# Optimization experiments

Hardware: AMD Instinct MI355X
Metric: run time of the kernel (lower is better)

Reference implementation:

```python
import jax, jax.numpy as jnp
import numpy as np

NUM_HEADS = 8      # in_channels // num_head_channels = 512 // 64
NUM_GROUPS = 32    # GroupNorm groups
EPS = 1e-5


def setup_inputs() -> dict:
    key = jax.random.key(0)
    ks = jax.random.split(key, 6)
    C = 512
    x = jax.random.normal(ks[0], (8, C, 32, 32), dtype=jnp.float32)
    gn_w = jax.random.normal(ks[1], (C,), dtype=jnp.float32) * 0.1 + 1.0
    gn_b = jax.random.normal(ks[2], (C,), dtype=jnp.float32) * 0.1
    qkv_w = jax.random.normal(ks[3], (3 * C, C), dtype=jnp.float32) / np.sqrt(C)
    qkv_b = jnp.zeros((3 * C,), dtype=jnp.float32)
    # NOTE: original zero-initializes to_out; we use small random weights so the
    # attention path contributes to the output (math is identical).
    out_w = jax.random.normal(ks[4], (C, C), dtype=jnp.float32) * 0.02
    out_b = jax.random.normal(ks[5], (C,), dtype=jnp.float32) * 0.02
    return {"x": x, "gn_w": gn_w, "gn_b": gn_b, "qkv_w": qkv_w,
            "qkv_b": qkv_b, "out_w": out_w, "out_b": out_b}


def _group_norm(net, gn_w, gn_b):
    b, c, t = net.shape
    g = net.reshape(b, NUM_GROUPS, c // NUM_GROUPS, t)
    mu = jnp.mean(g, axis=(2, 3), keepdims=True)
    var = jnp.var(g, axis=(2, 3), keepdims=True)
    n = ((g - mu) * jax.lax.rsqrt(var + EPS)).reshape(b, c, t)
    return n * gn_w[None, :, None] + gn_b[None, :, None]


def reference(x, gn_w, gn_b, qkv_w, qkv_b, out_w, out_b):
    b, c, h, w = x.shape
    area = h * w
    inp = x.reshape(b, c, area)                      # [b, c, t]
    n = _group_norm(inp, gn_w, gn_b)
    # 1x1 conv1d == channel GEMM
    qkv = jnp.einsum('oc,bct->bot', qkv_w, n) + qkv_b[None, :, None]  # [b, 3c, t]
    hd = c // NUM_HEADS
    # split_qkv_after_heads: view(b*H, 3*hd, area) then split along channel
    qkv = qkv.reshape(b * NUM_HEADS, 3 * hd, area)
    q, k, v = qkv[:, :hd], qkv[:, hd:2 * hd], qkv[:, 2 * hd:]
    scale = 1.0 / np.sqrt(np.sqrt(hd))               # sqrt-sqrt per-tensor scale
    attn = jnp.einsum('bct,bcs->bts', q * scale, k * scale)  # [bH, t, s]
    prob = jax.nn.softmax(attn, axis=-1)
    net = jnp.einsum('bts,bcs->bct', prob, v).reshape(b, c, area)
    out = jnp.einsum('oc,bct->bot', out_w, net) + out_b[None, :, None]
    return (inp + out).reshape(b, c, h, w)
```

## Files before the change

### kernel.cpp

```cpp
#include <hip/hip_runtime.h>
#include <hip/hip_bf16.h>

typedef __bf16 bf16_t;
typedef __bf16 bf16x8 __attribute__((ext_vector_type(8)));
typedef __bf16 bf16x4 __attribute__((ext_vector_type(4)));
typedef short  s16x4  __attribute__((ext_vector_type(4)));
typedef float  f32x4  __attribute__((ext_vector_type(4)));

#define B_DIM 8
#define C_DIM 512
#define T_DIM 1024
#define NH 8
#define HD 64

#define QSCALE 0.180336880111112f

__device__ __forceinline__ f32x4 mfma16_bf16(bf16x4 a, bf16x4 b, f32x4 c) {
    return __builtin_amdgcn_mfma_f32_16x16x16bf16_1k(
        __builtin_bit_cast(s16x4, a), __builtin_bit_cast(s16x4, b), c, 0, 0, 0);
}

__device__ __forceinline__ void block_sync_lds() {
    asm volatile("s_waitcnt lgkmcnt(0)" ::: "memory");
    __builtin_amdgcn_s_barrier();
}

__global__ __launch_bounds__(256) void gn_kernel(const float* __restrict__ x,
                                                 const float* __restrict__ gw,
                                                 const float* __restrict__ gb,
                                                 bf16_t* __restrict__ n_t,
                                                 const float* __restrict__ w1,
                                                 const float* __restrict__ w2,
                                                 bf16_t* __restrict__ o1,
                                                 bf16_t* __restrict__ o2)
{
    __shared__ bf16_t sX[16384];
    __shared__ float sred[8];
    int tid = threadIdx.x;

    if (blockIdx.x >= 256) {
        int tid2 = (blockIdx.x - 256) * 256 + tid;
        for (int p = 0; p < 16; ++p) {
            int q = tid2 + p * 16384;
            const f32x4* src;
            bf16x4* dst;
            int qq;
            if (q < 196608) { src = (const f32x4*)w1; dst = (bf16x4*)o1; qq = q; }
            else            { src = (const f32x4*)w2; dst = (bf16x4*)o2; qq = q - 196608; }
            f32x4 f = src[qq];
            bf16x4 h;
            for (int j = 0; j < 4; ++j) h[j] = (bf16_t)f[j];
            dst[qq] = h;
        }
        return;
    }

    int bb  = blockIdx.x >> 5;
    int g   = blockIdx.x & 31;
    const f32x4* xg4 = reinterpret_cast<const f32x4*>(x + (size_t)(bb * C_DIM + g * 16) * T_DIM);

    float s = 0.f, sq = 0.f;
    for (int i = 0; i < 16; ++i) {
        int v = tid + i * 256;
        f32x4 f = xg4[v];
        bf16x4 h;
        for (int j = 0; j < 4; ++j) {
            s += f[j]; sq += f[j] * f[j];
            h[j] = (bf16_t)f[j];
        }
        *reinterpret_cast<bf16x4*>(sX + v * 4) = h;
    }
    for (int off = 1; off < 64; off <<= 1) {
        s  += __shfl_xor(s, off);
        sq += __shfl_xor(sq, off);
    }
    int wv = tid >> 6;
    if ((tid & 63) == 0) { sred[wv * 2] = s; sred[wv * 2 + 1] = sq; }
    __syncthreads();
    s  = sred[0] + sred[2] + sred[4] + sred[6];
    sq = sred[1] + sred[3] + sred[5] + sred[7];
    float mean = s * (1.f / 16384.f);
    float var  = sq * (1.f / 16384.f) - mean * mean;
    float rs   = rsqrtf(var + 1e-5f);

    int hf = tid & 1;
    float aa[8], bbias[8];
    for (int j = 0; j < 8; ++j) {
        int c = hf * 8 + j;
        float av = gw[g * 16 + c] * rs;
        aa[j] = av;
        bbias[j] = gb[g * 16 + c] - mean * av;
    }
    bf16_t* ob = n_t + (size_t)bb * T_DIM * C_DIM + g * 16 + hf * 8;
    for (int p = 0; p < 8; ++p) {
        int t = (tid >> 1) + p * 128;
        bf16x8 o;
        for (int j = 0; j < 8; ++j) {
            float xv = (float)sX[(hf * 8 + j) * 1024 + t];
            o[j] = (bf16_t)(xv * aa[j] + bbias[j]);
        }
        *reinterpret_cast<bf16x8*>(ob + (size_t)t * C_DIM) = o;
    }
}

__global__ __launch_bounds__(256, 4) void qkv_gemm_kernel(
    const bf16_t* __restrict__ wqb, const float* __restrict__ bq,
    const bf16_t* __restrict__ n_t, bf16_t* __restrict__ qkv)
{
    __shared__ bf16_t sA[128 * 72];
    __shared__ bf16_t sB[128 * 72];
    int tid = threadIdx.x;
    int w = tid >> 6, lane = tid & 63, quad = lane >> 4, l15 = lane & 15;
    int bx = blockIdx.x;
    int t0 = blockIdx.y * 128;
    int bb = blockIdx.z;
    int o0 = bx * 128;
    const bf16_t* Ab = wqb + (size_t)o0 * C_DIM;
    const bf16_t* Bb = n_t + ((size_t)bb * T_DIM + t0) * C_DIM;

    f32x4 acc[4][4];
    for (int mt = 0; mt < 4; ++mt)
        for (int nt = 0; nt < 4; ++nt)
            acc[mt][nt] = f32x4{0.f, 0.f, 0.f, 0.f};
    int mw0 = (w >> 1) * 64;
    int nw0 = (w & 1) * 64;

    for (int k0 = 0; k0 < C_DIM; k0 += 64) {
        for (int i = 0; i < 4; ++i) {
            int v = tid + i * 256;
            int row = v >> 3, c8 = v & 7;
            *reinterpret_cast<bf16x8*>(sA + row * 72 + c8 * 8) =
                *reinterpret_cast<const bf16x8*>(Ab + (size_t)row * C_DIM + k0 + c8 * 8);
        }
        for (int i = 0; i < 4; ++i) {
            int v = tid + i * 256;
            int row = v >> 3, c8 = v & 7;
            *reinterpret_cast<bf16x8*>(sB + row * 72 + c8 * 8) =
                *reinterpret_cast<const bf16x8*>(Bb + (size_t)row * C_DIM + k0 + c8 * 8);
        }
        __syncthreads();
        for (int kk = 0; kk < 2; ++kk) {
            bf16x8 af[4], bfr[4];
            for (int mt = 0; mt < 4; ++mt)
                af[mt] = *reinterpret_cast<const bf16x8*>(sA + (mw0 + mt * 16 + l15) * 72 + kk * 32 + quad * 8);
            for (int nt = 0; nt < 4; ++nt)
                bfr[nt] = *reinterpret_cast<const bf16x8*>(sB + (nw0 + nt * 16 + l15) * 72 + kk * 32 + quad * 8);
            for (int mt = 0; mt < 4; ++mt)
                for (int nt = 0; nt < 4; ++nt)
                    acc[mt][nt] = __builtin_amdgcn_mfma_f32_16x16x32_bf16(af[mt], bfr[nt], acc[mt][nt], 0, 0, 0);
        }
        __syncthreads();
    }

    for (int half = 0; half < 2; ++half) {
        int chunk = bx * 2 + half;
        int h = chunk / 3, type = chunk % 3;
        size_t base = ((size_t)(bb * NH + h) * 3 + type) * (64 * 1024);
        bool mine = (mw0 >> 6) == half;

        if (type < 2) {
            float scl = (type == 0) ? QSCALE : 1.0f;
            if (mine)
                for (int mt = 0; mt < 4; ++mt)
                    for (int nt = 0; nt < 4; ++nt)
                        for (int r = 0; r < 4; ++r) {
                            int mw = mt * 16 + quad * 4 + r;
                            int tl = nw0 + nt * 16 + l15;
                            float v = (acc[mt][nt][r] + bq[o0 + half * 64 + mw]) * scl;
                            sB[tl * 72 + mw] = (bf16_t)v;
                        }
            __syncthreads();
            for (int i = 0; i < 4; ++i) {
                int v = tid + i * 256;
                int tl = v >> 3, c8 = v & 7;
                bf16x8 d = *reinterpret_cast<const bf16x8*>(sB + tl * 72 + c8 * 8);
                *reinterpret_cast<bf16x8*>(qkv + base + (size_t)(t0 + tl) * 64 + c8 * 8) = d;
            }
            __syncthreads();
        } else {
            if (mine)
                for (int mt = 0; mt < 4; ++mt)
                    for (int nt = 0; nt < 4; ++nt)
                        for (int r = 0; r < 4; ++r) {
                            int mw = mt * 16 + quad * 4 + r;
                            int tl = nw0 + nt * 16 + l15;
                            float v = acc[mt][nt][r] + bq[o0 + half * 64 + mw];
                            sB[mw * 136 + tl] = (bf16_t)v;
                        }
            __syncthreads();
            for (int i = 0; i < 4; ++i) {
                int v = tid + i * 256;
                int cc = v >> 4, t8 = (v & 15) * 8;
                bf16x8 d = *reinterpret_cast<const bf16x8*>(sB + cc * 136 + t8);
                *reinterpret_cast<bf16x8*>(qkv + base + (size_t)cc * 1024 + t0 + t8) = d;
            }
            __syncthreads();
        }
    }
}

__global__ __launch_bounds__(256, 2) void attn_kernel(const bf16_t* __restrict__ qkv,
                                                      bf16_t* __restrict__ net_t)
{
    __shared__ bf16_t sK[4][64 * 72];
    __shared__ bf16_t sV[4][64 * 72];
    int tid = threadIdx.x;
    int w = tid >> 6, lane = tid & 63, quad = lane >> 4, l15 = lane & 15;
    int bh = blockIdx.x;
    int qt = blockIdx.y;
    size_t qb = (size_t)bh * 3 * 65536;
    const bf16_t* Qg = qkv + qb + (size_t)qt * 8192;
    const bf16_t* Kg = qkv + qb + 65536;
    const bf16_t* Vg = qkv + qb + 2 * 65536;

    bf16x8 qf[2][2];
    for (int tt = 0; tt < 2; ++tt)
        for (int kk = 0; kk < 2; ++kk)
            qf[tt][kk] = *reinterpret_cast<const bf16x8*>(
                Qg + (size_t)(tt * 64 + w * 16 + l15) * 64 + kk * 32 + quad * 8);

    int vrow = tid >> 3;
    int vcol = (tid & 7) * 8;

    bf16x8 kA[2], vA[2], kB[2], vB[2];

    auto load_tiles = [&](bf16x8* kr, bf16x8* vr, int s0) {
        for (int i = 0; i < 2; ++i) {
            int r = vrow + i * 32;
            kr[i] = *reinterpret_cast<const bf16x8*>(Kg + (size_t)(s0 + r) * 64 + vcol);
            vr[i] = *reinterpret_cast<const bf16x8*>(Vg + (size_t)r * 1024 + s0 + vcol);
        }
    };
    auto write_tiles = [&](bf16_t* sKb, bf16_t* sVb, const bf16x8* kr, const bf16x8* vr) {
        for (int i = 0; i < 2; ++i) {
            int r = vrow + i * 32;
            *reinterpret_cast<bf16x8*>(sKb + r * 72 + vcol) = kr[i];
            *reinterpret_cast<bf16x8*>(sVb + r * 72 + vcol) = vr[i];
        }
    };

    f32x4 O0[4], O1[4];
    for (int i = 0; i < 4; ++i) {
        O0[i] = f32x4{0.f, 0.f, 0.f, 0.f};
        O1[i] = f32x4{0.f, 0.f, 0.f, 0.f};
    }
    f32x4 L0 = f32x4{0.f, 0.f, 0.f, 0.f};
    f32x4 L1 = f32x4{0.f, 0.f, 0.f, 0.f};
    const bf16x4 kONES = bf16x4{(bf16_t)1.f, (bf16_t)1.f, (bf16_t)1.f, (bf16_t)1.f};

    auto compute_tile = [&](const bf16_t* sKb, const bf16_t* sVb) {
        __builtin_amdgcn_s_setprio(1);
        for (int mt = 0; mt < 4; ++mt) {
            const bf16_t* krow = sKb + (mt * 16 + l15) * 72 + quad * 8;
            bf16x8 kf0 = *reinterpret_cast<const bf16x8*>(krow);
            bf16x8 kf1 = *reinterpret_cast<const bf16x8*>(krow + 32);
            f32x4 S0 = f32x4{0.f, 0.f, 0.f, 0.f};
            f32x4 S1 = f32x4{0.f, 0.f, 0.f, 0.f};
            S0 = __builtin_amdgcn_mfma_f32_16x16x32_bf16(kf0, qf[0][0], S0, 0, 0, 0);
            S1 = __builtin_amdgcn_mfma_f32_16x16x32_bf16(kf0, qf[1][0], S1, 0, 0, 0);
            S0 = __builtin_amdgcn_mfma_f32_16x16x32_bf16(kf1, qf[0][1], S0, 0, 0, 0);
            S1 = __builtin_amdgcn_mfma_f32_16x16x32_bf16(kf1, qf[1][1], S1, 0, 0, 0);
            bf16x4 pf0, pf1;
            for (int r = 0; r < 4; ++r) {
                pf0[r] = (bf16_t)__builtin_amdgcn_exp2f(S0[r]);
                pf1[r] = (bf16_t)__builtin_amdgcn_exp2f(S1[r]);
            }
            L0 = mfma16_bf16(kONES, pf0, L0);
            L1 = mfma16_bf16(kONES, pf1, L1);
            for (int ct = 0; ct < 4; ++ct) {
                bf16x4 vf = *reinterpret_cast<const bf16x4*>(sVb + (ct * 16 + l15) * 72 + mt * 16 + quad * 4);
                O0[ct] = mfma16_bf16(vf, pf0, O0[ct]);
                O1[ct] = mfma16_bf16(vf, pf1, O1[ct]);
            }
        }
        __builtin_amdgcn_s_setprio(0);
    };

    load_tiles(kA, vA, 0);
    load_tiles(kB, vB, 64);
    write_tiles(sK[0], sV[0], kA, vA);
    write_tiles(sK[1], sV[1], kB, vB);
    load_tiles(kA, vA, 128);
    load_tiles(kB, vB, 192);
    block_sync_lds();

    for (int ep = 0; ep < 4; ++ep) {
        write_tiles(sK[2], sV[2], kA, vA);
        write_tiles(sK[3], sV[3], kB, vB);
        if (ep < 3) {
            load_tiles(kA, vA, (4 * ep + 4) * 64);
            load_tiles(kB, vB, (4 * ep + 5) * 64);
        }
        compute_tile(sK[0], sV[0]);
        compute_tile(sK[1], sV[1]);
        block_sync_lds();
        if (ep < 3) {
            write_tiles(sK[0], sV[0], kA, vA);
            write_tiles(sK[1], sV[1], kB, vB);
            load_tiles(kA, vA, (4 * ep + 6) * 64);
            load_tiles(kB, vB, (4 * ep + 7) * 64);
        }
        compute_tile(sK[2], sV[2]);
        compute_tile(sK[3], sV[3]);
        if (ep < 3) block_sync_lds();
    }

    float inv0 = 1.f / L0[0];
    float inv1 = 1.f / L1[0];

    int bb = bh >> 3, h = bh & 7;
    int tbase = qt * 128 + w * 16 + l15;
    bf16_t* orow0 = net_t + ((size_t)bb * T_DIM + tbase) * C_DIM + h * 64;
    bf16_t* orow1 = net_t + ((size_t)bb * T_DIM + tbase + 64) * C_DIM + h * 64;
    for (int ct = 0; ct < 4; ++ct) {
        bf16x4 o4, o5;
        for (int r = 0; r < 4; ++r) {
            o4[r] = (bf16_t)(O0[ct][r] * inv0);
            o5[r] = (bf16_t)(O1[ct][r] * inv1);
        }
        *reinterpret_cast<bf16x4*>(orow0 + ct * 16 + quad * 4) = o4;
        *reinterpret_cast<bf16x4*>(orow1 + ct * 16 + quad * 4) = o5;
    }
}

__global__ __launch_bounds__(256) void out_gemm_kernel(
    const bf16_t* __restrict__ wob, const float* __restrict__ bo,
    const bf16_t* __restrict__ net_t, const float* __restrict__ x,
    float* __restrict__ out)
{
    __shared__ bf16_t sA[64 * 72];
    __shared__ bf16_t sB[128 * 72];
    int tid = threadIdx.x;
    int w = tid >> 6, lane = tid & 63, quad = lane >> 4, l15 = lane & 15;
    int o0 = blockIdx.x * 64;
    int t0 = blockIdx.y * 128;
    int bb = blockIdx.z;
    const bf16_t* Ab = wob + (size_t)o0 * C_DIM;
    const bf16_t* Bb = net_t + ((size_t)bb * T_DIM + t0) * C_DIM;

    f32x4 acc[2][4];
    for (int mt = 0; mt < 2; ++mt)
        for (int nt = 0; nt < 4; ++nt)
            acc[mt][nt] = f32x4{0.f, 0.f, 0.f, 0.f};
    int mw0 = (w >> 1) * 32;
    int nw0 = (w & 1) * 64;

    for (int k0 = 0; k0 < C_DIM; k0 += 64) {
        for (int i = 0; i < 2; ++i) {
            int v = tid + i * 256;
            int row = v >> 3, c8 = v & 7;
            *reinterpret_cast<bf16x8*>(sA + row * 72 + c8 * 8) =
                *reinterpret_cast<const bf16x8*>(Ab + (size_t)row * C_DIM + k0 + c8 * 8);
        }
        for (int i = 0; i < 4; ++i) {
            int v = tid + i * 256;
            int row = v >> 3, c8 = v & 7;
            *reinterpret_cast<bf16x8*>(sB + row * 72 + c8 * 8) =
                *reinterpret_cast<const bf16x8*>(Bb + (size_t)row * C_DIM + k0 + c8 * 8);
        }
        __syncthreads();
        for (int kk = 0; kk < 2; ++kk) {
            bf16x8 af[2], bfr[4];
            for (int mt = 0; mt < 2; ++mt)
                af[mt] = *reinterpret_cast<const bf16x8*>(sA + (mw0 + mt * 16 + l15) * 72 + kk * 32 + quad * 8);
            for (int nt = 0; nt < 4; ++nt)
                bfr[nt] = *reinterpret_cast<const bf16x8*>(sB + (nw0 + nt * 16 + l15) * 72 + kk * 32 + quad * 8);
            for (int mt = 0; mt < 2; ++mt)
                for (int nt = 0; nt < 4; ++nt)
                    acc[mt][nt] = __builtin_amdgcn_mfma_f32_16x16x32_bf16(af[mt], bfr[nt], acc[mt][nt], 0, 0, 0);
        }
        __syncthreads();
    }

    for (int mt = 0; mt < 2; ++mt)
        for (int nt = 0; nt < 4; ++nt)
            for (int r = 0; r < 4; ++r) {
                int o = o0 + mw0 + mt * 16 + quad * 4 + r;
                int t = t0 + nw0 + nt * 16 + l15;
                size_t idx = ((size_t)bb * C_DIM + o) * T_DIM + t;
                out[idx] = acc[mt][nt][r] + bo[o] + x[idx];
            }
}

extern "C" void kernel_launch(void* const* d_in, const int* in_sizes, int n_in,
                              void* d_out, int out_size, void* d_ws, size_t ws_size,
                              hipStream_t stream)
{
    const float* x     = (const float*)d_in[0];
    const float* gn_w  = (const float*)d_in[1];
    const float* gn_b  = (const float*)d_in[2];
    const float* qkv_w = (const float*)d_in[3];
    const float* qkv_b = (const float*)d_in[4];
    const float* out_w = (const float*)d_in[5];
    const float* out_b = (const float*)d_in[6];
    float* out = (float*)d_out;

    char* ws = (char*)d_ws;
    bf16_t* n_t   = (bf16_t*)(ws);
    bf16_t* qkv   = (bf16_t*)(ws + 8388608);
    bf16_t* net_t = (bf16_t*)(ws + 33554432);
    bf16_t* wqb   = (bf16_t*)(ws + 41943040);
    bf16_t* wob   = (bf16_t*)(ws + 41943040 + 1572864);

    gn_kernel<<<dim3(320), 256, 0, stream>>>(x, gn_w, gn_b, n_t, qkv_w, out_w, wqb, wob);
    qkv_gemm_kernel<<<dim3(12, 8, 8), 256, 0, stream>>>(wqb, qkv_b, n_t, qkv);
    attn_kernel<<<dim3(64, 8), 256, 0, stream>>>(qkv, net_t);
    out_gemm_kernel<<<dim3(8, 8, 8), 256, 0, stream>>>(wob, out_b, net_t, x, out);
}
```

Baseline: 149.7 us.

## Load GEMM tiles directly into LDS with XOR-swizzled layout

New measurement: 145.8 us, median of 2. -2.6%, faster.

```diff
diff --git a/kernel.cpp b/kernel.cpp
--- a/kernel.cpp
+++ b/kernel.cpp
@@ -15,6 +15,9 @@
 
 #define QSCALE 0.180336880111112f
 
+#define GAS __attribute__((address_space(1)))
+#define LAS __attribute__((address_space(3)))
+
 __device__ __forceinline__ f32x4 mfma16_bf16(bf16x4 a, bf16x4 b, f32x4 c) {
     return __builtin_amdgcn_mfma_f32_16x16x16bf16_1k(
         __builtin_bit_cast(s16x4, a), __builtin_bit_cast(s16x4, b), c, 0, 0, 0);
@@ -23,6 +26,16 @@
 __device__ __forceinline__ void block_sync_lds() {
     asm volatile("s_waitcnt lgkmcnt(0)" ::: "memory");
     __builtin_amdgcn_s_barrier();
+}
+
+__device__ __forceinline__ void stage_sync() {
+    asm volatile("s_waitcnt vmcnt(0)" ::: "memory");
+    __builtin_amdgcn_s_barrier();
+    asm volatile("" ::: "memory");
+}
+
+__device__ __forceinline__ void gload_lds16(const bf16_t* g, bf16_t* l) {
+    __builtin_amdgcn_global_load_lds((const GAS void*)g, (LAS void*)l, 16, 0, 0);
 }
 
 __global__ __launch_bounds__(256) void gn_kernel(const float* __restrict__ x,
@@ -107,8 +120,9 @@
     const bf16_t* __restrict__ wqb, const float* __restrict__ bq,
     const bf16_t* __restrict__ n_t, bf16_t* __restrict__ qkv)
 {
-    __shared__ bf16_t sA[128 * 72];
-    __shared__ bf16_t sB[128 * 72];
+    __shared__ __align__(16) bf16_t smem[16384];
+    bf16_t* sA = smem;
+    bf16_t* sB = smem + 8192;
     int tid = threadIdx.x;
     int w = tid >> 6, lane = tid & 63, quad = lane >> 4, l15 = lane & 15;
     int bx = blockIdx.x;
@@ -125,33 +139,39 @@
     int mw0 = (w >> 1) * 64;
     int nw0 = (w & 1) * 64;
 
+    int srow = (lane >> 3);
+    int scol = ((lane & 7) ^ srow) * 8;
+
     for (int k0 = 0; k0 < C_DIM; k0 += 64) {
         for (int i = 0; i < 4; ++i) {
-            int v = tid + i * 256;
-            int row = v >> 3, c8 = v & 7;
-            *reinterpret_cast<bf16x8*>(sA + row * 72 + c8 * 8) =
-                *reinterpret_cast<const bf16x8*>(Ab + (size_t)row * C_DIM + k0 + c8 * 8);
+            int row = i * 32 + w * 8 + srow;
+            gload_lds16(Ab + (size_t)row * C_DIM + k0 + scol, sA + i * 2048 + w * 512);
         }
         for (int i = 0; i < 4; ++i) {
-            int v = tid + i * 256;
-            int row = v >> 3, c8 = v & 7;
-            *reinterpret_cast<bf16x8*>(sB + row * 72 + c8 * 8) =
-                *reinterpret_cast<const bf16x8*>(Bb + (size_t)row * C_DIM + k0 + c8 * 8);
-        }
-        __syncthreads();
+            int row = i * 32 + w * 8 + srow;
+            gload_lds16(Bb + (size_t)row * C_DIM + k0 + scol, sB + i * 2048 + w * 512);
+        }
+        stage_sync();
         for (int kk = 0; kk < 2; ++kk) {
             bf16x8 af[4], bfr[4];
-            for (int mt = 0; mt < 4; ++mt)
-                af[mt] = *reinterpret_cast<const bf16x8*>(sA + (mw0 + mt * 16 + l15) * 72 + kk * 32 + quad * 8);
-            for (int nt = 0; nt < 4; ++nt)
-                bfr[nt] = *reinterpret_cast<const bf16x8*>(sB + (nw0 + nt * 16 + l15) * 72 + kk * 32 + quad * 8);
+            for (int mt = 0; mt < 4; ++mt) {
+                int row = mw0 + mt * 16 + l15;
+                int cs = kk * 4 + quad;
+                af[mt] = *reinterpret_cast<const bf16x8*>(sA + row * 64 + ((cs ^ (row & 7)) << 3));
+            }
+            for (int nt = 0; nt < 4; ++nt) {
+                int row = nw0 + nt * 16 + l15;
+                int cs = kk * 4 + quad;
+                bfr[nt] = *reinterpret_cast<const bf16x8*>(sB + row * 64 + ((cs ^ (row & 7)) << 3));
+            }
             for (int mt = 0; mt < 4; ++mt)
                 for (int nt = 0; nt < 4; ++nt)
                     acc[mt][nt] = __builtin_amdgcn_mfma_f32_16x16x32_bf16(af[mt], bfr[nt], acc[mt][nt], 0, 0, 0);
         }
-        __syncthreads();
-    }
-
+        __builtin_amdgcn_s_barrier();
+    }
+
+    bf16_t* es = smem;
     for (int half = 0; half < 2; ++half) {
         int chunk = bx * 2 + half;
         int h = chunk / 3, type = chunk % 3;
@@ -167,13 +187,13 @@
                             int mw = mt * 16 + quad * 4 + r;
                             int tl = nw0 + nt * 16 + l15;
                             float v = (acc[mt][nt][r] + bq[o0 + half * 64 + mw]) * scl;
-                            sB[tl * 72 + mw] = (bf16_t)v;
+                            es[tl * 72 + mw] = (bf16_t)v;
                         }
             __syncthreads();
             for (int i = 0; i < 4; ++i) {
                 int v = tid + i * 256;
                 int tl = v >> 3, c8 = v & 7;
-                bf16x8 d = *reinterpret_cast<const bf16x8*>(sB + tl * 72 + c8 * 8);
+                bf16x8 d = *reinterpret_cast<const bf16x8*>(es + tl * 72 + c8 * 8);
                 *reinterpret_cast<bf16x8*>(qkv + base + (size_t)(t0 + tl) * 64 + c8 * 8) = d;
             }
             __syncthreads();
@@ -185,13 +205,13 @@
                             int mw = mt * 16 + quad * 4 + r;
                             int tl = nw0 + nt * 16 + l15;
                             float v = acc[mt][nt][r] + bq[o0 + half * 64 + mw];
-                            sB[mw * 136 + tl] = (bf16_t)v;
+                            es[mw * 136 + tl] = (bf16_t)v;
                         }
             __syncthreads();
             for (int i = 0; i < 4; ++i) {
                 int v = tid + i * 256;
                 int cc = v >> 4, t8 = (v & 15) * 8;
-                bf16x8 d = *reinterpret_cast<const bf16x8*>(sB + cc * 136 + t8);
+                bf16x8 d = *reinterpret_cast<const bf16x8*>(es + cc * 136 + t8);
                 *reinterpret_cast<bf16x8*>(qkv + base + (size_t)cc * 1024 + t0 + t8) = d;
             }
             __syncthreads();
@@ -328,8 +348,9 @@
     const bf16_t* __restrict__ net_t, const float* __restrict__ x,
     float* __restrict__ out)
 {
-    __shared__ bf16_t sA[64 * 72];
-    __shared__ bf16_t sB[128 * 72];
+    __shared__ __align__(16) bf16_t smem[12288];
+    bf16_t* sA = smem;
+    bf16_t* sB = smem + 4096;
     int tid = threadIdx.x;
     int w = tid >> 6, lane = tid & 63, quad = lane >> 4, l15 = lane & 15;
     int o0 = blockIdx.x * 64;
@@ -345,31 +366,36 @@
     int mw0 = (w >> 1) * 32;
     int nw0 = (w & 1) * 64;
 
+    int srow = (lane >> 3);
+    int scol = ((lane & 7) ^ srow) * 8;
+
     for (int k0 = 0; k0 < C_DIM; k0 += 64) {
         for (int i = 0; i < 2; ++i) {
-            int v = tid + i * 256;
-            int row = v >> 3, c8 = v & 7;
-            *reinterpret_cast<bf16x8*>(sA + row * 72 + c8 * 8) =
-                *reinterpret_cast<const bf16x8*>(Ab + (size_t)row * C_DIM + k0 + c8 * 8);
+            int row = i * 32 + w * 8 + srow;
+            gload_lds16(Ab + (size_t)row * C_DIM + k0 + scol, sA + i * 2048 + w * 512);
         }
         for (int i = 0; i < 4; ++i) {
-            int v = tid + i * 256;
-            int row = v >> 3, c8 = v & 7;
-            *reinterpret_cast<bf16x8*>(sB + row * 72 + c8 * 8) =
-                *reinterpret_cast<const bf16x8*>(Bb + (size_t)row * C_DIM + k0 + c8 * 8);
-        }
-        __syncthreads();
+            int row = i * 32 + w * 8 + srow;
+            gload_lds16(Bb + (size_t)row * C_DIM + k0 + scol, sB + i * 2048 + w * 512);
+        }
+        stage_sync();
         for (int kk = 0; kk < 2; ++kk) {
             bf16x8 af[2], bfr[4];
-            for (int mt = 0; mt < 2; ++mt)
-                af[mt] = *reinterpret_cast<const bf16x8*>(sA + (mw0 + mt * 16 + l15) * 72 + kk * 32 + quad * 8);
-            for (int nt = 0; nt < 4; ++nt)
-                bfr[nt] = *reinterpret_cast<const bf16x8*>(sB + (nw0 + nt * 16 + l15) * 72 + kk * 32 + quad * 8);
+            for (int mt = 0; mt < 2; ++mt) {
+                int row = mw0 + mt * 16 + l15;
+                int cs = kk * 4 + quad;
+                af[mt] = *reinterpret_cast<const bf16x8*>(sA + row * 64 + ((cs ^ (row & 7)) << 3));
+            }
+            for (int nt = 0; nt < 4; ++nt) {
+                int row = nw0 + nt * 16 + l15;
+                int cs = kk * 4 + quad;
+                bfr[nt] = *reinterpret_cast<const bf16x8*>(sB + row * 64 + ((cs ^ (row & 7)) << 3));
+            }
             for (int mt = 0; mt < 2; ++mt)
                 for (int nt = 0; nt < 4; ++nt)
                     acc[mt][nt] = __builtin_amdgcn_mfma_f32_16x16x32_bf16(af[mt], bfr[nt], acc[mt][nt], 0, 0, 0);
         }
-        __syncthreads();
+        __builtin_amdgcn_s_barrier();
     }
 
     for (int mt = 0; mt < 2; ++mt)
```
